# Performance work log

Hardware: AMD Instinct MI355X
Metric: run time of the kernel (lower is better)

Reference implementation:

```python
import jax, jax.numpy as jnp
import numpy as np

N_NODES = 50000
DEG = 32
N_EDGES = N_NODES * DEG
IN_DIM = 256
HID = 64
OUT = 64
N_CLASSES = 40
N_GRAPHS = 64
NEG_SLOPE = 0.2


def setup_inputs() -> dict:
    key = jax.random.key(0)
    ks = jax.random.split(key, 12)
    h = jax.random.normal(ks[0], (N_NODES, IN_DIM), dtype=jnp.float32)
    # every node has exactly DEG incoming edges -> dst sorted, no zero in-degree
    dst = jnp.repeat(jnp.arange(N_NODES, dtype=jnp.int32), DEG)
    src = jax.random.randint(ks[1], (N_EDGES,), 0, N_NODES, dtype=jnp.int32)
    # evenly sized graphs so mean_nodes never divides by zero
    graph_ids = (jnp.arange(N_NODES, dtype=jnp.int32) * N_GRAPHS) // N_NODES
    s1 = 1.0 / np.sqrt(IN_DIM)
    s2 = 1.0 / np.sqrt(HID)
    W1 = jax.random.normal(ks[2], (IN_DIM, HID), jnp.float32) * s1
    al1 = jax.random.normal(ks[3], (HID,), jnp.float32) * s2
    ar1 = jax.random.normal(ks[4], (HID,), jnp.float32) * s2
    b1 = jnp.zeros((HID,), jnp.float32)
    W2 = jax.random.normal(ks[5], (HID, OUT), jnp.float32) * s2
    al2 = jax.random.normal(ks[6], (OUT,), jnp.float32) / np.sqrt(OUT)
    ar2 = jax.random.normal(ks[7], (OUT,), jnp.float32) / np.sqrt(OUT)
    b2 = jnp.zeros((OUT,), jnp.float32)
    p_drop = jnp.full((HID,), 0.5, jnp.float32)  # VariationalDropout retain probs
    Wc = jax.random.normal(ks[8], (OUT, N_CLASSES), jnp.float32) / np.sqrt(OUT)
    bc = jnp.zeros((N_CLASSES,), jnp.float32)
    return {"h": h, "src": src, "dst": dst, "graph_ids": graph_ids,
            "n_graphs": N_GRAPHS, "W1": W1, "al1": al1, "ar1": ar1, "b1": b1,
            "W2": W2, "al2": al2, "ar2": ar2, "b2": b2,
            "p_drop": p_drop, "Wc": Wc, "bc": bc}


def _gat_conv(h, W, al, ar, b, src, dst, n_nodes):
    f = h @ W                                  # [N, d]
    el = f @ al                                # [N]
    er = f @ ar                                # [N]
    e = jax.nn.leaky_relu(el[src] + er[dst], NEG_SLOPE)   # [E]
    m = jax.ops.segment_max(e, dst, num_segments=n_nodes, indices_are_sorted=True)
    ex = jnp.exp(e - m[dst])
    s = jax.ops.segment_sum(ex, dst, num_segments=n_nodes, indices_are_sorted=True)
    alpha = ex / s[dst]                        # edge softmax over incoming edges
    out = jax.ops.segment_sum(alpha[:, None] * f[src], dst,
                              num_segments=n_nodes, indices_are_sorted=True)
    return out + b


def reference(h, src, dst, graph_ids, n_graphs, W1, al1, ar1, b1,
              W2, al2, ar2, b2, p_drop, Wc, bc):
    n_nodes = h.shape[0]
    x = jax.nn.elu(_gat_conv(h, W1, al1, ar1, b1, src, dst, n_nodes))
    x = x * jnp.clip(p_drop, 0.0, 1.0)[None, :]          # deterministic var-dropout
    x = _gat_conv(x, W2, al2, ar2, b2, src, dst, n_nodes)
    # dgl.mean_nodes
    sums = jax.ops.segment_sum(x, graph_ids, num_segments=n_graphs, indices_are_sorted=True)
    cnts = jax.ops.segment_sum(jnp.ones((n_nodes,), x.dtype), graph_ids,
                               num_segments=n_graphs, indices_are_sorted=True)
    hg = sums / cnts[:, None]
    return hg @ Wc + bc
```

## Files before the change

### kernel.cpp

```cpp
#include <hip/hip_runtime.h>
#include <hip/hip_bf16.h>

#define N_NODES   50000
#define DEG       32
#define IN_DIM    256
#define HID       64
#define OUTD      64
#define N_CLASSES 40
#define N_GRAPHS  64

__device__ __forceinline__ float readlane_f(float v, int l) {
  return __uint_as_float(__builtin_amdgcn_readlane(__float_as_uint(v), l));
}

__device__ __forceinline__ unsigned short f2bf(float f) {
  unsigned int u = __float_as_uint(f);
  return (unsigned short)((u + 0x7fffu + ((u >> 16) & 1u)) >> 16);
}

__device__ __forceinline__ float2 bf2_to_f2(unsigned int v) {
  float2 r;
  r.x = __uint_as_float(v << 16);
  r.y = __uint_as_float(v & 0xffff0000u);
  return r;
}

template<int K_DIM>
__global__ __launch_bounds__(256, 2)
void gemm_heads_kernel(const float* __restrict__ A, const float* __restrict__ W,
                       const float* __restrict__ al, const float* __restrict__ ar,
                       unsigned short* __restrict__ Fb, float* __restrict__ el,
                       float* __restrict__ er, int n_rows)
{
  constexpr int BM = 128;
  constexpr int BK = 64;
  __shared__ float hT[BK][BM + 4];
  __shared__ float Wt[BK][OUTD + 4];

  const int tx   = threadIdx.x;
  const int rg   = tx >> 4;
  const int cg   = tx & 15;
  const int row0 = blockIdx.x * BM;

  float acc[8][4];
  #pragma unroll
  for (int r = 0; r < 8; ++r)
    #pragma unroll
    for (int c = 0; c < 4; ++c) acc[r][c] = 0.f;

  const int r_st = tx >> 1;
  const int kq0  = (tx & 1) * 8;

  for (int ck = 0; ck < K_DIM / BK; ++ck) {
    const int grow = row0 + r_st;
    #pragma unroll
    for (int i = 0; i < 8; ++i) {
      const int kq = kq0 + i;
      float4 v = make_float4(0.f, 0.f, 0.f, 0.f);
      if (grow < n_rows)
        v = *reinterpret_cast<const float4*>(&A[(long)grow * K_DIM + ck * BK + kq * 4]);
      hT[kq * 4 + 0][r_st] = v.x;
      hT[kq * 4 + 1][r_st] = v.y;
      hT[kq * 4 + 2][r_st] = v.z;
      hT[kq * 4 + 3][r_st] = v.w;
    }
    #pragma unroll
    for (int i = 0; i < 4; ++i) {
      const int j  = tx + 256 * i;
      const int k  = j >> 4;
      const int c4 = j & 15;
      *reinterpret_cast<float4*>(&Wt[k][c4 * 4]) =
          *reinterpret_cast<const float4*>(&W[(long)(ck * BK + k) * OUTD + c4 * 4]);
    }
    __syncthreads();

    #pragma unroll 8
    for (int kk = 0; kk < BK; ++kk) {
      const float4 a0 = *reinterpret_cast<const float4*>(&hT[kk][rg * 8]);
      const float4 a1 = *reinterpret_cast<const float4*>(&hT[kk][rg * 8 + 4]);
      const float4 b  = *reinterpret_cast<const float4*>(&Wt[kk][cg * 4]);
      const float av[8] = {a0.x, a0.y, a0.z, a0.w, a1.x, a1.y, a1.z, a1.w};
      const float bv[4] = {b.x, b.y, b.z, b.w};
      #pragma unroll
      for (int r = 0; r < 8; ++r)
        #pragma unroll
        for (int c = 0; c < 4; ++c)
          acc[r][c] = fmaf(av[r], bv[c], acc[r][c]);
    }
    __syncthreads();
  }

  float al4[4], ar4[4];
  #pragma unroll
  for (int c = 0; c < 4; ++c) { al4[c] = al[cg * 4 + c]; ar4[c] = ar[cg * 4 + c]; }

  float pe[8], pr[8];
  #pragma unroll
  for (int r = 0; r < 8; ++r) {
    const int row = row0 + rg * 8 + r;
    pe[r] = acc[r][0] * al4[0] + acc[r][1] * al4[1] + acc[r][2] * al4[2] + acc[r][3] * al4[3];
    pr[r] = acc[r][0] * ar4[0] + acc[r][1] * ar4[1] + acc[r][2] * ar4[2] + acc[r][3] * ar4[3];
    if (row < n_rows) {
      ushort4 o;
      o.x = f2bf(acc[r][0]); o.y = f2bf(acc[r][1]);
      o.z = f2bf(acc[r][2]); o.w = f2bf(acc[r][3]);
      *reinterpret_cast<ushort4*>(&Fb[(long)row * 64 + cg * 4]) = o;
    }
  }

  float* pel = &hT[0][0];
  float* per = pel + 128 * 17;
  #pragma unroll
  for (int r = 0; r < 8; ++r) {
    pel[(rg * 8 + r) * 17 + cg] = pe[r];
    per[(rg * 8 + r) * 17 + cg] = pr[r];
  }
  __syncthreads();
  if (tx < 128) {
    float se = 0.f, sr = 0.f;
    #pragma unroll
    for (int j = 0; j < 16; ++j) { se += pel[tx * 17 + j]; sr += per[tx * 17 + j]; }
    const int row = row0 + tx;
    if (row < n_rows) { el[row] = se; er[row] = sr; }
  }
}

template<int MODE>
__global__ __launch_bounds__(256)
void agg_kernel(const unsigned int* __restrict__ F2,
                const float* __restrict__ el, const float* __restrict__ er,
                const int* __restrict__ src, const float* __restrict__ bias,
                const float* __restrict__ pd, float* __restrict__ X, int n_pairs)
{
  const int wid  = (blockIdx.x * 256 + threadIdx.x) >> 6;
  const int lane = threadIdx.x & 63;
  if (wid >= n_pairs) return;
  const int half = lane >> 5;
  const int l32  = lane & 31;
  const int node = wid * 2 + half;

  const int s = src[wid * 64 + lane];
  float ev = el[s] + er[node];
  ev = ev > 0.f ? ev : 0.2f * ev;

  float m = ev;
  #pragma unroll
  for (int d = 16; d; d >>= 1) m = fmaxf(m, __shfl_xor(m, d));
  const float p = __expf(ev - m);
  float sum = p;
  #pragma unroll
  for (int d = 16; d; d >>= 1) sum += __shfl_xor(sum, d);
  const float alpha = p / sum;

  float ax = 0.f, ay = 0.f;
  #pragma unroll
  for (int t = 0; t < 32; ++t) {
    const int   svA = __builtin_amdgcn_readlane(s, t);
    const int   svB = __builtin_amdgcn_readlane(s, t + 32);
    const float aA  = readlane_f(alpha, t);
    const float aB  = readlane_f(alpha, t + 32);
    const int   sv  = half ? svB : svA;
    const float av  = half ? aB : aA;
    const float2 vf = bf2_to_f2(F2[(long)sv * 32 + l32]);
    ax = fmaf(av, vf.x, ax);
    ay = fmaf(av, vf.y, ay);
  }

  float ox = ax + bias[l32 * 2];
  float oy = ay + bias[l32 * 2 + 1];
  if (MODE == 1) {
    ox = ox > 0.f ? ox : (__expf(ox) - 1.f);
    oy = oy > 0.f ? oy : (__expf(oy) - 1.f);
    ox *= fminf(fmaxf(pd[l32 * 2], 0.f), 1.f);
    oy *= fminf(fmaxf(pd[l32 * 2 + 1], 0.f), 1.f);
  }
  reinterpret_cast<float2*>(X)[(long)node * 32 + l32] = make_float2(ox, oy);
}

__global__ __launch_bounds__(256)
void partial_pool_kernel(const float* __restrict__ X2, float* __restrict__ sums)
{
  const int wv   = (blockIdx.x * 256 + threadIdx.x) >> 6;
  const int lane = threadIdx.x & 63;
  if (wv >= N_NODES / 16) return;
  const int base = wv * 16;

  float accR = 0.f;
  int   gcur = (base * 64) / N_NODES;
  #pragma unroll 4
  for (int n = 0; n < 16; ++n) {
    const int i = base + n;
    const int g = (i * 64) / N_NODES;
    if (g != gcur) {
      atomicAdd(&sums[gcur * 64 + lane], accR);
      accR = 0.f; gcur = g;
    }
    accR += X2[(long)i * 64 + lane];
  }
  atomicAdd(&sums[gcur * 64 + lane], accR);
}

__global__ __launch_bounds__(64)
void classify_kernel(const float* __restrict__ sums, const float* __restrict__ Wc,
                     const float* __restrict__ bc, float* __restrict__ out)
{
  const int g     = blockIdx.x;
  const int start = (g * N_NODES + N_GRAPHS - 1) / N_GRAPHS;
  const int end   = ((g + 1) * N_NODES + N_GRAPHS - 1) / N_GRAPHS;
  const int t     = threadIdx.x;

  __shared__ float hg[64];
  hg[t] = sums[g * 64 + t] / (float)(end - start);
  __syncthreads();
  if (t < N_CLASSES) {
    float o = bc[t];
    #pragma unroll
    for (int j = 0; j < 64; ++j) o = fmaf(hg[j], Wc[j * N_CLASSES + t], o);
    out[g * N_CLASSES + t] = o;
  }
}

extern "C" void kernel_launch(void* const* d_in, const int* in_sizes, int n_in,
                              void* d_out, int out_size, void* d_ws, size_t ws_size,
                              hipStream_t stream)
{
  const float* h   = (const float*)d_in[0];
  const int*   src = (const int*)d_in[1];
  const float* W1  = (const float*)d_in[5];
  const float* al1 = (const float*)d_in[6];
  const float* ar1 = (const float*)d_in[7];
  const float* b1  = (const float*)d_in[8];
  const float* W2  = (const float*)d_in[9];
  const float* al2 = (const float*)d_in[10];
  const float* ar2 = (const float*)d_in[11];
  const float* b2  = (const float*)d_in[12];
  const float* pd  = (const float*)d_in[13];
  const float* Wc  = (const float*)d_in[14];
  const float* bc  = (const float*)d_in[15];
  float* out = (float*)d_out;

  float*          ws   = (float*)d_ws;
  float*          xbuf = ws;
  unsigned short* Fb   = (unsigned short*)(ws + 3200000);
  float*          elb  = ws + 4800000;
  float*          erb  = elb + 50000;
  float*          sums = erb + 50000;

  hipMemsetAsync(sums, 0, N_GRAPHS * 64 * sizeof(float), stream);

  gemm_heads_kernel<IN_DIM><<<(N_NODES + 127) / 128, 256, 0, stream>>>(
      h, W1, al1, ar1, Fb, elb, erb, N_NODES);
  agg_kernel<1><<<(N_NODES / 2) / 4, 256, 0, stream>>>(
      (const unsigned int*)Fb, elb, erb, src, b1, pd, xbuf, N_NODES / 2);

  gemm_heads_kernel<HID><<<(N_NODES + 127) / 128, 256, 0, stream>>>(
      xbuf, W2, al2, ar2, Fb, elb, erb, N_NODES);
  agg_kernel<2><<<(N_NODES / 2) / 4, 256, 0, stream>>>(
      (const unsigned int*)Fb, elb, erb, src, b2, pd, xbuf, N_NODES / 2);

  partial_pool_kernel<<<(N_NODES / 16 + 3) / 4, 256, 0, stream>>>(xbuf, sums);
  classify_kernel<<<N_GRAPHS, 64, 0, stream>>>(sums, Wc, bc, out);
}
```

Measured before the change: 219.6 us.

## Replace FP32 SIMT GEMM with bf16 MFMA GEMM for node projections

Rewrites the per-layer feature projection kernel to use 16x16x32 bf16 MFMA instructions. Each wave computes a 16-row tile and reads A directly from global memory, converting it to bf16 in registers. W is staged in LDS as transposed bf16. The el/er attention heads are reduced with cross-lane shuffles instead of an LDS pass. This cuts the FP32 FMA compute cost of the first GEMM, at the price of bf16 rounding of the inputs and weights, smaller tiles, and less coalesced A loads.

```diff
diff --git a/kernel.cpp b/kernel.cpp
--- a/kernel.cpp
+++ b/kernel.cpp
@@ -9,6 +9,9 @@
 #define N_CLASSES 40
 #define N_GRAPHS  64
 
+typedef __attribute__((ext_vector_type(8))) short bf16x8;
+typedef __attribute__((ext_vector_type(4))) float f32x4;
+
 __device__ __forceinline__ float readlane_f(float v, int l) {
   return __uint_as_float(__builtin_amdgcn_readlane(__float_as_uint(v), l));
 }
@@ -26,102 +29,92 @@
 }
 
 template<int K_DIM>
-__global__ __launch_bounds__(256, 2)
-void gemm_heads_kernel(const float* __restrict__ A, const float* __restrict__ W,
-                       const float* __restrict__ al, const float* __restrict__ ar,
-                       unsigned short* __restrict__ Fb, float* __restrict__ el,
-                       float* __restrict__ er, int n_rows)
-{
-  constexpr int BM = 128;
-  constexpr int BK = 64;
-  __shared__ float hT[BK][BM + 4];
-  __shared__ float Wt[BK][OUTD + 4];
-
-  const int tx   = threadIdx.x;
-  const int rg   = tx >> 4;
-  const int cg   = tx & 15;
-  const int row0 = blockIdx.x * BM;
-
-  float acc[8][4];
-  #pragma unroll
-  for (int r = 0; r < 8; ++r)
-    #pragma unroll
-    for (int c = 0; c < 4; ++c) acc[r][c] = 0.f;
-
-  const int r_st = tx >> 1;
-  const int kq0  = (tx & 1) * 8;
-
-  for (int ck = 0; ck < K_DIM / BK; ++ck) {
-    const int grow = row0 + r_st;
-    #pragma unroll
-    for (int i = 0; i < 8; ++i) {
-      const int kq = kq0 + i;
-      float4 v = make_float4(0.f, 0.f, 0.f, 0.f);
-      if (grow < n_rows)
-        v = *reinterpret_cast<const float4*>(&A[(long)grow * K_DIM + ck * BK + kq * 4]);
-      hT[kq * 4 + 0][r_st] = v.x;
-      hT[kq * 4 + 1][r_st] = v.y;
-      hT[kq * 4 + 2][r_st] = v.z;
-      hT[kq * 4 + 3][r_st] = v.w;
-    }
-    #pragma unroll
-    for (int i = 0; i < 4; ++i) {
-      const int j  = tx + 256 * i;
-      const int k  = j >> 4;
-      const int c4 = j & 15;
-      *reinterpret_cast<float4*>(&Wt[k][c4 * 4]) =
-          *reinterpret_cast<const float4*>(&W[(long)(ck * BK + k) * OUTD + c4 * 4]);
-    }
-    __syncthreads();
-
-    #pragma unroll 8
-    for (int kk = 0; kk < BK; ++kk) {
-      const float4 a0 = *reinterpret_cast<const float4*>(&hT[kk][rg * 8]);
-      const float4 a1 = *reinterpret_cast<const float4*>(&hT[kk][rg * 8 + 4]);
-      const float4 b  = *reinterpret_cast<const float4*>(&Wt[kk][cg * 4]);
-      const float av[8] = {a0.x, a0.y, a0.z, a0.w, a1.x, a1.y, a1.z, a1.w};
-      const float bv[4] = {b.x, b.y, b.z, b.w};
-      #pragma unroll
-      for (int r = 0; r < 8; ++r)
-        #pragma unroll
-        for (int c = 0; c < 4; ++c)
-          acc[r][c] = fmaf(av[r], bv[c], acc[r][c]);
-    }
-    __syncthreads();
-  }
-
-  float al4[4], ar4[4];
-  #pragma unroll
-  for (int c = 0; c < 4; ++c) { al4[c] = al[cg * 4 + c]; ar4[c] = ar[cg * 4 + c]; }
-
-  float pe[8], pr[8];
-  #pragma unroll
-  for (int r = 0; r < 8; ++r) {
-    const int row = row0 + rg * 8 + r;
-    pe[r] = acc[r][0] * al4[0] + acc[r][1] * al4[1] + acc[r][2] * al4[2] + acc[r][3] * al4[3];
-    pr[r] = acc[r][0] * ar4[0] + acc[r][1] * ar4[1] + acc[r][2] * ar4[2] + acc[r][3] * ar4[3];
-    if (row < n_rows) {
-      ushort4 o;
-      o.x = f2bf(acc[r][0]); o.y = f2bf(acc[r][1]);
-      o.z = f2bf(acc[r][2]); o.w = f2bf(acc[r][3]);
-      *reinterpret_cast<ushort4*>(&Fb[(long)row * 64 + cg * 4]) = o;
-    }
-  }
-
-  float* pel = &hT[0][0];
-  float* per = pel + 128 * 17;
-  #pragma unroll
-  for (int r = 0; r < 8; ++r) {
-    pel[(rg * 8 + r) * 17 + cg] = pe[r];
-    per[(rg * 8 + r) * 17 + cg] = pr[r];
+__global__ __launch_bounds__(256)
+void gemm_heads_mfma(const float* __restrict__ A, const float* __restrict__ W,
+                     const float* __restrict__ al, const float* __restrict__ ar,
+                     unsigned short* __restrict__ Fb, float* __restrict__ el,
+                     float* __restrict__ er, int n_rows)
+{
+  constexpr int KP = K_DIM + 8;
+  __shared__ __align__(16) unsigned short Wt[64 * KP];
+
+  {
+    constexpr int ITER = K_DIM * 64 / 1024;
+    #pragma unroll
+    for (int i = 0; i < ITER; ++i) {
+      const int idx4 = threadIdx.x * 4 + i * 1024;
+      const int k = idx4 >> 6;
+      const int c = idx4 & 63;
+      const float4 w = *reinterpret_cast<const float4*>(&W[idx4]);
+      Wt[(c + 0) * KP + k] = f2bf(w.x);
+      Wt[(c + 1) * KP + k] = f2bf(w.y);
+      Wt[(c + 2) * KP + k] = f2bf(w.z);
+      Wt[(c + 3) * KP + k] = f2bf(w.w);
+    }
   }
   __syncthreads();
-  if (tx < 128) {
-    float se = 0.f, sr = 0.f;
-    #pragma unroll
-    for (int j = 0; j < 16; ++j) { se += pel[tx * 17 + j]; sr += per[tx * 17 + j]; }
-    const int row = row0 + tx;
-    if (row < n_rows) { el[row] = se; er[row] = sr; }
+
+  const int lane = threadIdx.x & 63;
+  const int wv   = threadIdx.x >> 6;
+  const int c    = lane & 15;
+  const int g    = lane >> 4;
+  const int row0 = blockIdx.x * 64 + wv * 16;
+
+  const long arow = min(row0 + c, n_rows - 1);
+  const int  kq   = g * 8;
+
+  f32x4 acc[4];
+  #pragma unroll
+  for (int nt = 0; nt < 4; ++nt) acc[nt] = (f32x4){0.f, 0.f, 0.f, 0.f};
+
+  #pragma unroll
+  for (int ks = 0; ks < K_DIM / 32; ++ks) {
+    const float4 q0 = *reinterpret_cast<const float4*>(&A[arow * K_DIM + ks * 32 + kq]);
+    const float4 q1 = *reinterpret_cast<const float4*>(&A[arow * K_DIM + ks * 32 + kq + 4]);
+    union { bf16x8 v; unsigned short u[8]; } af;
+    af.u[0] = f2bf(q0.x); af.u[1] = f2bf(q0.y); af.u[2] = f2bf(q0.z); af.u[3] = f2bf(q0.w);
+    af.u[4] = f2bf(q1.x); af.u[5] = f2bf(q1.y); af.u[6] = f2bf(q1.z); af.u[7] = f2bf(q1.w);
+    #pragma unroll
+    for (int nt = 0; nt < 4; ++nt) {
+      const bf16x8 bf =
+          *reinterpret_cast<const bf16x8*>(&Wt[(nt * 16 + c) * KP + ks * 32 + kq]);
+      acc[nt] = __builtin_amdgcn_mfma_f32_16x16x32_bf16(af.v, bf, acc[nt], 0, 0, 0);
+    }
+  }
+
+  #pragma unroll
+  for (int nt = 0; nt < 4; ++nt) {
+    #pragma unroll
+    for (int r = 0; r < 4; ++r) {
+      const int row = row0 + g * 4 + r;
+      if (row < n_rows) Fb[(long)row * 64 + nt * 16 + c] = f2bf(acc[nt][r]);
+    }
+  }
+
+  float alc[4], arc[4];
+  #pragma unroll
+  for (int nt = 0; nt < 4; ++nt) { alc[nt] = al[nt * 16 + c]; arc[nt] = ar[nt * 16 + c]; }
+
+  float pe[4], pr[4];
+  #pragma unroll
+  for (int r = 0; r < 4; ++r) {
+    pe[r] = acc[0][r] * alc[0] + acc[1][r] * alc[1] + acc[2][r] * alc[2] + acc[3][r] * alc[3];
+    pr[r] = acc[0][r] * arc[0] + acc[1][r] * arc[1] + acc[2][r] * arc[2] + acc[3][r] * arc[3];
+  }
+  #pragma unroll
+  for (int d = 1; d < 16; d <<= 1) {
+    #pragma unroll
+    for (int r = 0; r < 4; ++r) {
+      pe[r] += __shfl_xor(pe[r], d);
+      pr[r] += __shfl_xor(pr[r], d);
+    }
+  }
+  if (c == 0) {
+    #pragma unroll
+    for (int r = 0; r < 4; ++r) {
+      const int row = row0 + g * 4 + r;
+      if (row < n_rows) { el[row] = pe[r]; er[row] = pr[r]; }
+    }
   }
 }
 
@@ -248,12 +241,12 @@
 
   hipMemsetAsync(sums, 0, N_GRAPHS * 64 * sizeof(float), stream);
 
-  gemm_heads_kernel<IN_DIM><<<(N_NODES + 127) / 128, 256, 0, stream>>>(
+  gemm_heads_mfma<IN_DIM><<<(N_NODES + 63) / 64, 256, 0, stream>>>(
       h, W1, al1, ar1, Fb, elb, erb, N_NODES);
   agg_kernel<1><<<(N_NODES / 2) / 4, 256, 0, stream>>>(
       (const unsigned int*)Fb, elb, erb, src, b1, pd, xbuf, N_NODES / 2);
 
-  gemm_heads_kernel<HID><<<(N_NODES + 127) / 128, 256, 0, stream>>>(
+  gemm_heads_mfma<HID><<<(N_NODES + 63) / 64, 256, 0, stream>>>(
       xbuf, W2, al2, ar2, Fb, elb, erb, N_NODES);
   agg_kernel<2><<<(N_NODES / 2) / 4, 256, 0, stream>>>(
       (const unsigned int*)Fb, elb, erb, src, b2, pd, xbuf, N_NODES / 2);
```

Result: faster. 198.8 us (-9.5%).
